# Optimization experiments

Measured on AMD Instinct MI355X. Metric: run time of the kernel, lower is better.

## Reference

```python
import jax, jax.numpy as jnp
import numpy as np
from jax.scipy.special import logsumexp

PAD, SOS, EOS = 0, 2, 3
V, E, H, L, K = 30000, 128, 256, 2, 32   # vocab, embed, hidden, lstm layers, tags
B, T = 64, 512
HP = H // L                               # per-direction hidden size (PyTorch: hidden_sz//num_layer)


def setup_inputs() -> dict:
    key = jax.random.key(0)
    ks = jax.random.split(key, 20)
    # sorted-descending lengths (pack_padded_sequence requirement)
    lengths = jnp.sort(jax.random.randint(ks[0], (B,), T // 2, T + 1))[::-1]
    pos = jnp.arange(T)
    valid = pos[None, :] < lengths[:, None]
    x = jnp.where(valid, jax.random.randint(ks[1], (B, T), 4, V), PAD)
    y = jax.random.randint(ks[2], (B, T + 1), 4, K).at[:, 0].set(SOS)
    embed = jax.random.normal(ks[3], (V, E)) * 0.1
    s = 1.0 / np.sqrt(HP)
    u = lambda k, shape: jax.random.uniform(k, shape, minval=-s, maxval=s)
    p = {}
    i = 4
    for l, din in [(0, E), (1, 2 * HP)]:
        for d in 'fb':
            p['wi_l%d%s' % (l, d)] = u(ks[i], (4 * HP, din)); i += 1
            p['wh_l%d%s' % (l, d)] = u(ks[i], (4 * HP, HP)); i += 1
            p['b_l%d%s' % (l, d)] = u(ks[i], (4 * HP,)); i += 1
    so = 1.0 / np.sqrt(H)
    w_out = jax.random.uniform(ks[i], (K, H), minval=-so, maxval=so); i += 1
    b_out = jax.random.uniform(ks[i], (K,), minval=-so, maxval=so); i += 1
    trans = jax.random.normal(ks[i], (K, K))
    trans = trans.at[SOS, :].set(-10000.0)
    trans = trans.at[:, EOS].set(-10000.0)
    trans = trans.at[:, PAD].set(-10000.0)
    trans = trans.at[PAD, :].set(-10000.0)
    trans = trans.at[PAD, EOS].set(0.0)
    trans = trans.at[PAD, PAD].set(0.0)
    return {'x': x, 'y': y, 'embed': embed, **p, 'w_out': w_out, 'b_out': b_out, 'trans': trans}


def _lstm_dir(xs, wi, wh, b):
    # xs: [T, B, D] -> hidden states [T, B, HP]; PyTorch gate order i, f, g, o
    bsz = xs.shape[1]
    def step(carry, xt):
        h, c = carry
        z = xt @ wi.T + h @ wh.T + b
        i, f, g, o = jnp.split(z, 4, axis=-1)
        c = jax.nn.sigmoid(f) * c + jax.nn.sigmoid(i) * jnp.tanh(g)
        h = jax.nn.sigmoid(o) * jnp.tanh(c)
        return (h, c), h
    init = (jnp.zeros((bsz, HP), xs.dtype), jnp.zeros((bsz, HP), xs.dtype))
    _, hs = jax.lax.scan(step, init, xs)
    return hs


def _flip(a, lengths):
    # per-sequence reversal of valid prefix (matches packed-sequence reverse LSTM)
    pos = jnp.arange(a.shape[1])
    idx = jnp.where(pos[None, :] < lengths[:, None], lengths[:, None] - 1 - pos[None, :], pos[None, :])
    return jnp.take_along_axis(a, idx[:, :, None], axis=1)


def _bilstm_layer(inp, lengths, wif, whf, bf, wib, whb, bb):
    hf = _lstm_dir(inp.swapaxes(0, 1), wif, whf, bf).swapaxes(0, 1)
    hb = _flip(_lstm_dir(_flip(inp, lengths).swapaxes(0, 1), wib, whb, bb).swapaxes(0, 1), lengths)
    return jnp.concatenate([hf, hb], axis=-1)


def _forward(x, y, embed, wi_l0f, wh_l0f, b_l0f, wi_l0b, wh_l0b, b_l0b,
             wi_l1f, wh_l1f, b_l1f, wi_l1b, wh_l1b, b_l1b, w_out, b_out, trans):
    mask = (x > PAD).astype(jnp.float32)          # [B, T]
    lengths = mask.sum(1).astype(jnp.int32)       # [B]
    h = embed[x]                                  # [B, T, E]
    h = _bilstm_layer(h, lengths, wi_l0f, wh_l0f, b_l0f, wi_l0b, wh_l0b, b_l0b)
    h = _bilstm_layer(h, lengths, wi_l1f, wh_l1f, b_l1f, wi_l1b, wh_l1b, b_l1b)
    h = jnp.einsum('btd,kd->btk', h, w_out) + b_out   # emissions [B, T, K]
    h = h * mask[:, :, None]
    bsz = x.shape[0]
    # CRF partition function: sequential log-sum-exp recurrence
    init = jnp.full((bsz, K), -10000.0).at[:, SOS].set(0.0)
    def step(score, tb):
        h_t, m_t = tb                              # [B, K], [B]
        s = logsumexp(score[:, None, :] + h_t[:, :, None] + trans[None, :, :], axis=-1)
        return jnp.where(m_t[:, None] > 0, s, score), None
    score, _ = jax.lax.scan(step, init, (h.swapaxes(0, 1), mask.T))
    logZ = logsumexp(score + trans[EOS], axis=-1)
    # gold path score
    emit = jnp.take_along_axis(h, y[:, 1:, None], axis=2)[..., 0]  # [B, T]
    tr = trans[y[:, 1:], y[:, :-1]]                                 # [B, T]
    gold = ((emit + tr) * mask).sum(1)
    last_tag = jnp.take_along_axis(y, lengths[:, None], axis=1)[:, 0]
    gold = gold + trans[EOS, last_tag]
    return logZ - gold                              # [B] negative log-likelihood


def reference(x, y, embed, wi_l0f, wh_l0f, b_l0f, wi_l0b, wh_l0b, b_l0b,
              wi_l1f, wh_l1f, b_l1f, wi_l1b, wh_l1b, b_l1b, w_out, b_out, trans):
    return _forward(x, y, embed, wi_l0f, wh_l0f, b_l0f, wi_l0b, wh_l0b, b_l0b,
                    wi_l1f, wh_l1f, b_l1f, wi_l1b, wh_l1b, b_l1b, w_out, b_out, trans)
```

## Files before the change

kernel.cpp:

```cpp
#include <hip/hip_runtime.h>

typedef _Float16 half_t;
typedef _Float16 half2_t __attribute__((ext_vector_type(2)));
typedef _Float16 half4_t __attribute__((ext_vector_type(4)));
typedef _Float16 half8_t __attribute__((ext_vector_type(8)));
typedef float float4_t __attribute__((ext_vector_type(4)));

#define BB 64
#define TT 512
#define EE 128
#define HPP 128
#define KK 32
#define MTOT (BB*TT)
#define NWID 1024

__device__ __forceinline__ void lds_barrier() {
    asm volatile("s_waitcnt lgkmcnt(0)\n\ts_barrier" ::: "memory");
}

__device__ __forceinline__ float fast_sigmoid(float x) {
    return __builtin_amdgcn_rcpf(1.f + __expf(-x));
}
__device__ __forceinline__ float fast_tanh(float x) {
    return 1.f - 2.f * __builtin_amdgcn_rcpf(__expf(2.f * x) + 1.f);
}

__global__ void k_lengths(const int* __restrict__ x, int* __restrict__ lens) {
    __shared__ int cnt;
    if (threadIdx.x == 0) cnt = 0;
    __syncthreads();
    int local = 0;
    for (int t = threadIdx.x; t < TT; t += blockDim.x)
        local += (x[blockIdx.x * TT + t] > 0) ? 1 : 0;
    atomicAdd(&cnt, local);
    __syncthreads();
    if (threadIdx.x == 0) lens[blockIdx.x] = cnt;
}

__global__ void k_pack(const float* __restrict__ wi0f, const float* __restrict__ wi0b,
                       const float* __restrict__ wi1f, const float* __restrict__ wi1b,
                       const float* __restrict__ w_out,
                       const int* __restrict__ x, const float* __restrict__ embed,
                       half_t* __restrict__ WP0, half_t* __restrict__ WP1,
                       half_t* __restrict__ WO, half_t* __restrict__ e16) {
    int idx = blockIdx.x * blockDim.x + threadIdx.x;
    int stride = gridDim.x * blockDim.x;
    const int n0 = NWID * EE;
    const int n1 = NWID * 256;
    for (int i = idx; i < n0; i += stride) {
        int j8 = i & 7; int ln = (i >> 3) & 63; int rest = i >> 9;
        int kc = rest & 3; int ntg = rest >> 2;
        int lr = ln & 15, lq = ln >> 4;
        int n = ntg * 16 + lr;
        int k = kc * 32 + lq * 8 + j8;
        float v = (n < 512) ? wi0f[n * 128 + k] : wi0b[(n - 512) * 128 + k];
        WP0[i] = (half_t)v;
    }
    for (int i = idx; i < n1; i += stride) {
        int j8 = i & 7; int ln = (i >> 3) & 63; int rest = i >> 9;
        int kc = rest & 7; int ntg = rest >> 3;
        int lr = ln & 15, lq = ln >> 4;
        int n = ntg * 16 + lr;
        int k = kc * 32 + lq * 8 + j8;
        float v = (n < 512) ? wi1f[n * 256 + k] : wi1b[(n - 512) * 256 + k];
        WP1[i] = (half_t)v;
    }
    for (int i = idx; i < KK * 256; i += stride)
        WO[i] = (half_t)w_out[i];
    for (int i = idx; i < MTOT * 16; i += stride) {
        int bt = i >> 4;
        int c  = (i & 15) * 8;
        int xi = x[bt];
        const float4* src = (const float4*)(embed + (size_t)xi * EE + c);
        float4 a = src[0], b = src[1];
        half8_t o;
        o[0] = (half_t)a.x; o[1] = (half_t)a.y; o[2] = (half_t)a.z; o[3] = (half_t)a.w;
        o[4] = (half_t)b.x; o[5] = (half_t)b.y; o[6] = (half_t)b.z; o[7] = (half_t)b.w;
        *(half8_t*)(e16 + (size_t)bt * EE + c) = o;
    }
}

__global__ __launch_bounds__(256) void k_gemm(const half_t* __restrict__ A,
                                              const half_t* __restrict__ WP,
                                              const float* __restrict__ bias_f,
                                              const float* __restrict__ bias_b,
                                              half_t* __restrict__ C, int Kd) {
    const int KC = Kd >> 5;
    int wave = threadIdx.x >> 6;
    int lane = threadIdx.x & 63;
    int m0 = blockIdx.x * 64 + wave * 16;
    int dir = blockIdx.y >> 1;
    int cg  = blockIdx.y & 1;
    int lr = lane & 15;
    int lq = lane >> 4;

    float4_t acc[16];
    #pragma unroll
    for (int i = 0; i < 16; i++) acc[i] = (float4_t){0.f, 0.f, 0.f, 0.f};

    const half_t* Arow  = A + (size_t)(m0 + lr) * Kd + lq * 8;
    const int ntile0 = dir * 32 + cg * 4;
    const half_t* Wbase = WP + ((size_t)ntile0 * KC * 64 + lane) * 8;

    for (int kc = 0; kc < KC; kc++) {
        half8_t af = *(const half8_t*)(Arow + kc * 32);
        #pragma unroll
        for (int nt = 0; nt < 16; nt++) {
            int g = nt >> 2, sub = nt & 3;
            half8_t bf = *(const half8_t*)(Wbase + (((size_t)(g * 8 + sub) * KC + kc) << 9));
            acc[nt] = __builtin_amdgcn_mfma_f32_16x16x32_f16(af, bf, acc[nt], 0, 0, 0);
        }
    }

    const float* bias = dir ? bias_b : bias_f;
    char* Crow = (char*)C + dir * 1024 + (size_t)(cg * 64) * 8;
    #pragma unroll
    for (int sub = 0; sub < 4; sub++) {
        int cbase = cg * 64 + sub * 16 + lr;
        float b0 = bias[cbase];
        float b1 = bias[128 + cbase];
        float b2 = bias[256 + cbase];
        float b3 = bias[384 + cbase];
        #pragma unroll
        for (int i = 0; i < 4; i++) {
            int m = m0 + lq * 4 + i;
            half4_t o;
            o[0] = (half_t)(acc[0 * 4 + sub][i] + b0);
            o[1] = (half_t)(acc[1 * 4 + sub][i] + b1);
            o[2] = (half_t)(acc[2 * 4 + sub][i] + b2);
            o[3] = (half_t)(acc[3 * 4 + sub][i] + b3);
            *(half4_t*)(Crow + (size_t)m * 2048 + (sub * 16 + lr) * 8) = o;
        }
    }
}

__global__ __launch_bounds__(512, 1) void k_lstm(const half_t* __restrict__ zbuf,
                                                 const float* __restrict__ wh_f,
                                                 const float* __restrict__ wh_b,
                                                 const int* __restrict__ lens,
                                                 half_t* __restrict__ hout) {
    const int grp  = blockIdx.x >> 1;
    const int dir  = blockIdx.x & 1;
    const int tid  = threadIdx.x;
    const int wv   = tid >> 6;
    const int lane = tid & 63;
    const int q    = lane >> 4;
    const int col  = lane & 15;
    const int s    = col & 3;
    const int ii   = col >> 2;
    const int b    = grp * 4 + s;
    const int Lb   = lens[b];
    const int maxL = lens[grp * 4];
    const float* wh = dir ? wh_b : wh_f;

    __shared__ half_t hb[2][512];

    half8_t a0[4], a1[4], a2[4], a3[4];
    #pragma unroll
    for (int i = 0; i < 4; i++) {
        int r = wv * 64 + i * 16 + col;
        int orow = (r & 3) * 128 + (r >> 2);
        #pragma unroll
        for (int ck = 0; ck < 4; ck++) {
            const float4* src = (const float4*)(wh + (size_t)orow * 128 + ck * 32 + q * 8);
            float4 f0 = src[0], f1 = src[1];
            half8_t h8;
            h8[0] = (half_t)f0.x; h8[1] = (half_t)f0.y; h8[2] = (half_t)f0.z; h8[3] = (half_t)f0.w;
            h8[4] = (half_t)f1.x; h8[5] = (half_t)f1.y; h8[6] = (half_t)f1.z; h8[7] = (half_t)f1.w;
            if (i == 0) a0[ck] = h8;
            else if (i == 1) a1[ck] = h8;
            else if (i == 2) a2[ck] = h8;
            else a3[ck] = h8;
        }
    }

    hb[0][tid] = (half_t)0.f;

    const int cell = wv * 16 + ii * 4 + q;
    const int woff = (cell >> 5) * 128 + (s * 4 + ((cell >> 3) & 3)) * 8 + (cell & 7);
    const int roff = (s * 4 + q) * 8;

    const bool s1 = (ii == 1), s2 = (ii == 2), s3 = (ii == 3);

    float c = 0.f;
    const char* zb8  = (const char*)zbuf + dir * 1024;
    char*       hob8 = (char*)hout + dir * 256;

    const int zdelta = dir ? -2048 : 2048;
    const int hdelta = dir ? -512 : 512;

    int t0 = dir ? (Lb - 1) : 0;
    int t1 = dir ? (Lb - 2) : 1;
    half4_t z1 = *(const half4_t*)(zb8 + (unsigned)((b * TT + t0) * 2048 + cell * 8));
    half4_t z2 = *(const half4_t*)(zb8 + (unsigned)((b * TT + t1) * 2048 + cell * 8));

    int zoff = (b * TT + (dir ? (Lb - 3) : 2)) * 2048 + cell * 8;
    int hoff = (b * TT + t0) * 512 + cell * 2;
    const unsigned deadoff = (unsigned)((b * TT + 511) * 512 + cell * 2);

    __syncthreads();

    const int maxL2 = (maxL + 1) & ~1;

#define LSTM_STEP(RB, ZC, T)                                                      \
    {                                                                             \
        half8_t bf0 = *(const half8_t*)&hb[RB][roff];                             \
        half8_t bf1 = *(const half8_t*)&hb[RB][128 + roff];                       \
        half8_t bf2 = *(const half8_t*)&hb[RB][256 + roff];                       \
        half8_t bf3 = *(const half8_t*)&hb[RB][384 + roff];                       \
        float4_t A0 = (float4_t){0.f, 0.f, 0.f, 0.f};                             \
        float4_t A1 = (float4_t){0.f, 0.f, 0.f, 0.f};                             \
        float4_t A2 = (float4_t){0.f, 0.f, 0.f, 0.f};                             \
        float4_t A3 = (float4_t){0.f, 0.f, 0.f, 0.f};                             \
        A0 = __builtin_amdgcn_mfma_f32_16x16x32_f16(a0[0], bf0, A0, 0, 0, 0);     \
        A1 = __builtin_amdgcn_mfma_f32_16x16x32_f16(a1[0], bf0, A1, 0, 0, 0);     \
        A2 = __builtin_amdgcn_mfma_f32_16x16x32_f16(a2[0], bf0, A2, 0, 0, 0);     \
        A3 = __builtin_amdgcn_mfma_f32_16x16x32_f16(a3[0], bf0, A3, 0, 0, 0);     \
        A0 = __builtin_amdgcn_mfma_f32_16x16x32_f16(a0[1], bf1, A0, 0, 0, 0);     \
        A1 = __builtin_amdgcn_mfma_f32_16x16x32_f16(a1[1], bf1, A1, 0, 0, 0);     \
        A2 = __builtin_amdgcn_mfma_f32_16x16x32_f16(a2[1], bf1, A2, 0, 0, 0);     \
        A3 = __builtin_amdgcn_mfma_f32_16x16x32_f16(a3[1], bf1, A3, 0, 0, 0);     \
        A0 = __builtin_amdgcn_mfma_f32_16x16x32_f16(a0[2], bf2, A0, 0, 0, 0);     \
        A1 = __builtin_amdgcn_mfma_f32_16x16x32_f16(a1[2], bf2, A1, 0, 0, 0);     \
        A2 = __builtin_amdgcn_mfma_f32_16x16x32_f16(a2[2], bf2, A2, 0, 0, 0);     \
        A3 = __builtin_amdgcn_mfma_f32_16x16x32_f16(a3[2], bf2, A3, 0, 0, 0);     \
        A0 = __builtin_amdgcn_mfma_f32_16x16x32_f16(a0[3], bf3, A0, 0, 0, 0);     \
        A1 = __builtin_amdgcn_mfma_f32_16x16x32_f16(a1[3], bf3, A1, 0, 0, 0);     \
        A2 = __builtin_amdgcn_mfma_f32_16x16x32_f16(a2[3], bf3, A2, 0, 0, 0);     \
        A3 = __builtin_amdgcn_mfma_f32_16x16x32_f16(a3[3], bf3, A3, 0, 0, 0);     \
        float g0 = s1 ? A1[0] : (s2 ? A2[0] : (s3 ? A3[0] : A0[0]));              \
        float g1 = s1 ? A1[1] : (s2 ? A2[1] : (s3 ? A3[1] : A0[1]));              \
        float g2 = s1 ? A1[2] : (s2 ? A2[2] : (s3 ? A3[2] : A0[2]));              \
        float g3 = s1 ? A1[3] : (s2 ? A2[3] : (s3 ? A3[3] : A0[3]));              \
        float zi = g0 + (float)ZC[0];                                             \
        float zf = g1 + (float)ZC[1];                                             \
        float zg = g2 + (float)ZC[2];                                             \
        float zo = g3 + (float)ZC[3];                                             \
        ZC = *(const half4_t*)(zb8 + (unsigned)zoff);         \
        zoff += zdelta;                                                           \
        zoff = zoff < 0 ? 0 : zoff;                                               \
        float si = fast_sigmoid(zi);                                              \
        float sf = fast_sigmoid(zf);                                              \
        float so = fast_sigmoid(zo);                                              \
        float tg = fast_tanh(zg);                                                 \
        c = sf * c + si * tg;                                                     \
        float th = fast_tanh(c);                                                  \
        half_t hh = (half_t)(so * th);                                            \
        hb[RB ^ 1][woff] = hh;                                                    \
        unsigned soff = ((T) < Lb) ? (unsigned)hoff : deadoff;                    \
        *(half_t*)(hob8 + soff) = hh;                        \
        hoff += hdelta;                                                           \
        lds_barrier();                                                            \
    }

    for (int t = 0; t < maxL2; t += 2) {
        LSTM_STEP(0, z1, t)
        LSTM_STEP(1, z2, t + 1)
    }
#undef LSTM_STEP
}

__global__ __launch_bounds__(256) void k_logits(const half_t* __restrict__ h1,
                                                const half_t* __restrict__ WO,
                                                const float* __restrict__ b_out,
                                                float* __restrict__ logits) {
    int wave = threadIdx.x >> 6;
    int lane = threadIdx.x & 63;
    int m0 = blockIdx.x * 64 + wave * 16;
    int lr = lane & 15;
    int lq = lane >> 4;

    float4_t acc0 = (float4_t){0.f, 0.f, 0.f, 0.f};
    float4_t acc1 = (float4_t){0.f, 0.f, 0.f, 0.f};

    const half_t* Arow = h1 + (size_t)(m0 + lr) * 256 + lq * 8;
    const half_t* Brow = WO + (size_t)lr * 256 + lq * 8;

    #pragma unroll
    for (int k = 0; k < 256; k += 32) {
        half8_t af = *(const half8_t*)(Arow + k);
        half8_t b0 = *(const half8_t*)(Brow + k);
        half8_t b1 = *(const half8_t*)(Brow + 16 * 256 + k);
        acc0 = __builtin_amdgcn_mfma_f32_16x16x32_f16(af, b0, acc0, 0, 0, 0);
        acc1 = __builtin_amdgcn_mfma_f32_16x16x32_f16(af, b1, acc1, 0, 0, 0);
    }
    #pragma unroll
    for (int nt = 0; nt < 2; nt++) {
        int n = nt * 16 + lr;
        float bias = b_out[n];
        #pragma unroll
        for (int i = 0; i < 4; i++) {
            int m = m0 + lq * 4 + i;
            logits[(size_t)m * KK + n] = (nt == 0 ? acc0[i] : acc1[i]) + bias;
        }
    }
}

__global__ __launch_bounds__(64) void k_crf(const float* __restrict__ logits,
                                            const float* __restrict__ trans,
                                            const int* __restrict__ y,
                                            const int* __restrict__ lens,
                                            float* __restrict__ out) {
    int b = blockIdx.x;
    int lane = threadIdx.x;
    int k = lane & 31;
    __shared__ float TR[32][33];
    __shared__ __align__(16) float PS[32];

    for (int i = lane; i < 1024; i += 64) TR[i >> 5][i & 31] = trans[i];

    float et[32];
    const float* trow = trans + k * 32;
    #pragma unroll
    for (int j = 0; j < 32; j++) et[j] = __expf(trow[j]);
    __syncthreads();

    int Lb = lens[b];
    const int* yb = y + b * (TT + 1);
    const float* lgb = logits + (size_t)(b * TT) * KK;

    float g = 0.f;
    for (int t = lane; t < Lb; t += 64) {
        int yt = yb[t], yt1 = yb[t + 1];
        g += lgb[(size_t)t * KK + yt1] + TR[yt1][yt];
    }
    #pragma unroll
    for (int s = 1; s < 64; s <<= 1) g += __shfl_xor(g, s);
    float gold = g + TR[3][yb[Lb]];

    float score = lgb[k] + TR[k][2];

    const float* lgp = lgb + KK + k;
    float lg_cur = *lgp;
    for (int t = 1; t < Lb; t++) {
        float lg_use = lg_cur;
        lgp += KK;
        lg_cur = *lgp;
        float m = __builtin_bit_cast(float, __builtin_amdgcn_readlane(__builtin_bit_cast(int, score), 4));
        float P = __expf(score - m);
        if (lane < 32) PS[k] = P;
        float4 ps[8];
        #pragma unroll
        for (int j = 0; j < 8; j++) ps[j] = *(const float4*)&PS[j * 4];
        const float* psf = (const float*)ps;
        float a0 = 0.f, a1 = 0.f, a2 = 0.f, a3 = 0.f;
        #pragma unroll
        for (int j = 0; j < 8; j++) {
            a0 = fmaf(et[j], psf[j], a0);
            a1 = fmaf(et[j + 8], psf[j + 8], a1);
            a2 = fmaf(et[j + 16], psf[j + 16], a2);
            a3 = fmaf(et[j + 24], psf[j + 24], a3);
        }
        score = lg_use + m + __logf((a0 + a1) + (a2 + a3));
    }

    float v = score + TR[3][k];
    float m2 = v;
    #pragma unroll
    for (int s = 1; s < 32; s <<= 1) m2 = fmaxf(m2, __shfl_xor(m2, s));
    float e = __expf(v - m2);
    #pragma unroll
    for (int s = 1; s < 32; s <<= 1) e += __shfl_xor(e, s);
    float logZ = m2 + __logf(e);

    if (lane == 0) out[b] = logZ - gold;
}

extern "C" void kernel_launch(void* const* d_in, const int* in_sizes, int n_in,
                              void* d_out, int out_size, void* d_ws, size_t ws_size,
                              hipStream_t stream) {
    const int*   x      = (const int*)d_in[0];
    const int*   y      = (const int*)d_in[1];
    const float* embed  = (const float*)d_in[2];
    const float* wi_l0f = (const float*)d_in[3];
    const float* wh_l0f = (const float*)d_in[4];
    const float* b_l0f  = (const float*)d_in[5];
    const float* wi_l0b = (const float*)d_in[6];
    const float* wh_l0b = (const float*)d_in[7];
    const float* b_l0b  = (const float*)d_in[8];
    const float* wi_l1f = (const float*)d_in[9];
    const float* wh_l1f = (const float*)d_in[10];
    const float* b_l1f  = (const float*)d_in[11];
    const float* wi_l1b = (const float*)d_in[12];
    const float* wh_l1b = (const float*)d_in[13];
    const float* b_l1b  = (const float*)d_in[14];
    const float* w_out  = (const float*)d_in[15];
    const float* b_out  = (const float*)d_in[16];
    const float* trans  = (const float*)d_in[17];
    float* out = (float*)d_out;

    char* base = (char*)d_ws;
    size_t off = 0;
    auto take = [&](size_t bytes) -> char* {
        char* r = base + off;
        off = (off + bytes + 255) & ~(size_t)255;
        return r;
    };
    half_t* zA  = (half_t*)take((size_t)MTOT * NWID * 2);
    half_t* h0  = (half_t*)take((size_t)MTOT * 256 * 2);
    half_t* h1  = (half_t*)take((size_t)MTOT * 256 * 2);
    half_t* e16 = (half_t*)take((size_t)MTOT * EE * 2);
    float*  lg  = (float*)take((size_t)MTOT * KK * 4);
    half_t* WP0 = (half_t*)take((size_t)NWID * EE * 2);
    half_t* WP1 = (half_t*)take((size_t)NWID * 256 * 2);
    half_t* WO  = (half_t*)take((size_t)KK * 256 * 2);
    int*    lens = (int*)take(BB * 4);

    k_lengths<<<BB, 256, 0, stream>>>(x, lens);
    k_pack<<<512, 256, 0, stream>>>(wi_l0f, wi_l0b, wi_l1f, wi_l1b, w_out, x, embed,
                                    WP0, WP1, WO, e16);
    k_gemm<<<dim3(MTOT / 64, 4), 256, 0, stream>>>(e16, WP0, b_l0f, b_l0b, zA, 128);
    k_lstm<<<32, 512, 0, stream>>>(zA, wh_l0f, wh_l0b, lens, h0);
    k_gemm<<<dim3(MTOT / 64, 4), 256, 0, stream>>>(h0, WP1, b_l1f, b_l1b, zA, 256);
    k_lstm<<<32, 512, 0, stream>>>(zA, wh_l1f, wh_l1b, lens, h1);
    k_logits<<<MTOT / 64, 256, 0, stream>>>(h1, WO, b_out, lg);
    k_crf<<<BB, 64, 0, stream>>>(lg, trans, y, lens, out);
}
```

Before: 914.9 us.

## Skip padded GEMM tiles, fold length count into pack, use readlane in CRF

Moves the per-sequence length computation into the pack kernel, which removes one launch. The input-projection GEMMs and the logits kernel now exit early for 64-row tiles that lie entirely past a sequence's length, which avoids work on padding. The CRF recurrence now broadcasts the exp-scores with readlane instead of an LDS round trip. Skipped tiles leave their outputs unwritten, so correctness depends on downstream kernels never reading padded positions. The pack kernel also reads lens from blocks 0-63 only, which relies on block ordering for nothing else.

```diff
diff --git a/kernel.cpp b/kernel.cpp
--- a/kernel.cpp
+++ b/kernel.cpp
@@ -24,17 +24,8 @@
 __device__ __forceinline__ float fast_tanh(float x) {
     return 1.f - 2.f * __builtin_amdgcn_rcpf(__expf(2.f * x) + 1.f);
 }
-
-__global__ void k_lengths(const int* __restrict__ x, int* __restrict__ lens) {
-    __shared__ int cnt;
-    if (threadIdx.x == 0) cnt = 0;
-    __syncthreads();
-    int local = 0;
-    for (int t = threadIdx.x; t < TT; t += blockDim.x)
-        local += (x[blockIdx.x * TT + t] > 0) ? 1 : 0;
-    atomicAdd(&cnt, local);
-    __syncthreads();
-    if (threadIdx.x == 0) lens[blockIdx.x] = cnt;
+__device__ __forceinline__ float readlane_f(float v, int lane) {
+    return __builtin_bit_cast(float, __builtin_amdgcn_readlane(__builtin_bit_cast(int, v), lane));
 }
 
 __global__ void k_pack(const float* __restrict__ wi0f, const float* __restrict__ wi0b,
@@ -42,7 +33,20 @@
                        const float* __restrict__ w_out,
                        const int* __restrict__ x, const float* __restrict__ embed,
                        half_t* __restrict__ WP0, half_t* __restrict__ WP1,
-                       half_t* __restrict__ WO, half_t* __restrict__ e16) {
+                       half_t* __restrict__ WO, half_t* __restrict__ e16,
+                       int* __restrict__ lens) {
+    if (blockIdx.x < BB) {
+        __shared__ int cnt;
+        if (threadIdx.x == 0) cnt = 0;
+        __syncthreads();
+        int local = 0;
+        for (int t = threadIdx.x; t < TT; t += blockDim.x)
+            local += (x[blockIdx.x * TT + t] > 0) ? 1 : 0;
+        atomicAdd(&cnt, local);
+        __syncthreads();
+        if (threadIdx.x == 0) lens[blockIdx.x] = cnt;
+    }
+
     int idx = blockIdx.x * blockDim.x + threadIdx.x;
     int stride = gridDim.x * blockDim.x;
     const int n0 = NWID * EE;
@@ -84,7 +88,12 @@
                                               const half_t* __restrict__ WP,
                                               const float* __restrict__ bias_f,
                                               const float* __restrict__ bias_b,
+                                              const int* __restrict__ lens,
                                               half_t* __restrict__ C, int Kd) {
+    {
+        int t0 = (blockIdx.x * 64) & 511;
+        if (t0 >= lens[blockIdx.x >> 3]) return;
+    }
     const int KC = Kd >> 5;
     int wave = threadIdx.x >> 6;
     int lane = threadIdx.x & 63;
@@ -263,7 +272,12 @@
 __global__ __launch_bounds__(256) void k_logits(const half_t* __restrict__ h1,
                                                 const half_t* __restrict__ WO,
                                                 const float* __restrict__ b_out,
+                                                const int* __restrict__ lens,
                                                 float* __restrict__ logits) {
+    {
+        int t0 = (blockIdx.x * 64) & 511;
+        if (t0 >= lens[blockIdx.x >> 3]) return;
+    }
     int wave = threadIdx.x >> 6;
     int lane = threadIdx.x & 63;
     int m0 = blockIdx.x * 64 + wave * 16;
@@ -305,7 +319,6 @@
     int lane = threadIdx.x;
     int k = lane & 31;
     __shared__ float TR[32][33];
-    __shared__ __align__(16) float PS[32];
 
     for (int i = lane; i < 1024; i += 64) TR[i >> 5][i & 31] = trans[i];
 
@@ -336,20 +349,15 @@
         float lg_use = lg_cur;
         lgp += KK;
         lg_cur = *lgp;
-        float m = __builtin_bit_cast(float, __builtin_amdgcn_readlane(__builtin_bit_cast(int, score), 4));
+        float m = readlane_f(score, 4);
         float P = __expf(score - m);
-        if (lane < 32) PS[k] = P;
-        float4 ps[8];
-        #pragma unroll
-        for (int j = 0; j < 8; j++) ps[j] = *(const float4*)&PS[j * 4];
-        const float* psf = (const float*)ps;
         float a0 = 0.f, a1 = 0.f, a2 = 0.f, a3 = 0.f;
         #pragma unroll
         for (int j = 0; j < 8; j++) {
-            a0 = fmaf(et[j], psf[j], a0);
-            a1 = fmaf(et[j + 8], psf[j + 8], a1);
-            a2 = fmaf(et[j + 16], psf[j + 16], a2);
-            a3 = fmaf(et[j + 24], psf[j + 24], a3);
+            a0 = fmaf(et[j],      readlane_f(P, j),      a0);
+            a1 = fmaf(et[j + 8],  readlane_f(P, j + 8),  a1);
+            a2 = fmaf(et[j + 16], readlane_f(P, j + 16), a2);
+            a3 = fmaf(et[j + 24], readlane_f(P, j + 24), a3);
         }
         score = lg_use + m + __logf((a0 + a1) + (a2 + a3));
     }
@@ -406,13 +414,12 @@
     half_t* WO  = (half_t*)take((size_t)KK * 256 * 2);
     int*    lens = (int*)take(BB * 4);
 
-    k_lengths<<<BB, 256, 0, stream>>>(x, lens);
     k_pack<<<512, 256, 0, stream>>>(wi_l0f, wi_l0b, wi_l1f, wi_l1b, w_out, x, embed,
-                                    WP0, WP1, WO, e16);
-    k_gemm<<<dim3(MTOT / 64, 4), 256, 0, stream>>>(e16, WP0, b_l0f, b_l0b, zA, 128);
+                                    WP0, WP1, WO, e16, lens);
+    k_gemm<<<dim3(MTOT / 64, 4), 256, 0, stream>>>(e16, WP0, b_l0f, b_l0b, lens, zA, 128);
     k_lstm<<<32, 512, 0, stream>>>(zA, wh_l0f, wh_l0b, lens, h0);
-    k_gemm<<<dim3(MTOT / 64, 4), 256, 0, stream>>>(h0, WP1, b_l1f, b_l1b, zA, 256);
+    k_gemm<<<dim3(MTOT / 64, 4), 256, 0, stream>>>(h0, WP1, b_l1f, b_l1b, lens, zA, 256);
     k_lstm<<<32, 512, 0, stream>>>(zA, wh_l1f, wh_l1b, lens, h1);
-    k_logits<<<MTOT / 64, 256, 0, stream>>>(h1, WO, b_out, lg);
+    k_logits<<<MTOT / 64, 256, 0, stream>>>(h1, WO, b_out, lens, lg);
     k_crf<<<BB, 64, 0, stream>>>(lg, trans, y, lens, out);
 }
```

Result: faster. 883.9 us (-3.4%).
